# Optimization experiments

Hardware: AMD Instinct MI355X
Metric: run time of the kernel (lower is better)

## Reference

```python
import jax, jax.numpy as jnp
import numpy as np

B, S, D, H = 8, 384, 768, 12
MAX_POS = 512
P = 2 * MAX_POS - 1  # 1023


def setup_inputs() -> dict:
    key = jax.random.key(0)
    ks = jax.random.split(key, 14)
    w = 0.02
    return {
        "x": jax.random.normal(ks[0], (B, S, D), jnp.float32),
        "rel_pos_emb": jax.random.normal(ks[1], (P, D), jnp.float32),
        "Wq": jax.random.normal(ks[2], (D, D), jnp.float32) * w,
        "bq": jax.random.normal(ks[3], (D,), jnp.float32) * w,
        "Wk": jax.random.normal(ks[4], (D, D), jnp.float32) * w,
        "bk": jax.random.normal(ks[5], (D,), jnp.float32) * w,
        "Wv": jax.random.normal(ks[6], (D, D), jnp.float32) * w,
        "bv": jax.random.normal(ks[7], (D,), jnp.float32) * w,
        "q_bias": jax.random.normal(ks[8], (D,), jnp.float32) * w,
        "v_bias": jax.random.normal(ks[9], (D,), jnp.float32) * w,
        "Wpk": jax.random.normal(ks[10], (D, D), jnp.float32) * w,
        "Wpq": jax.random.normal(ks[11], (D, D), jnp.float32) * w,
        "Wo": jax.random.normal(ks[12], (D, D), jnp.float32) * w,
        "bo": jax.random.normal(ks[13], (D,), jnp.float32) * w,
    }


def reference(x, rel_pos_emb, Wq, bq, Wk, bk, Wv, bv, q_bias, v_bias, Wpk, Wpq, Wo, bo):
    b, s, d = x.shape
    dh = d // H
    scale = dh ** -0.5
    # relative position index: rel[i, j] = j - i + MAX_POS - 1
    rel = (jnp.arange(s)[None, :] - jnp.arange(s)[:, None]) + MAX_POS - 1
    emb = rel_pos_emb[rel]                      # [S, S, D]
    q = (x @ Wq + bq + q_bias).reshape(b, s, H, dh)
    k = (x @ Wk + bk).reshape(b, s, H, dh)
    v = (x @ Wv + bv + v_bias).reshape(b, s, H, dh)
    Kp = (emb @ Wpk).reshape(s, s, H, dh)       # pos keys   [i, j, h, d]
    Qp = (emb @ Wpq).reshape(s, s, H, dh)       # pos queries[i, j, h, d]
    c2c = jnp.einsum('bihd,bjhd->bhij', q, k)
    c2p = jnp.einsum('bihd,ijhd->bhij', q, Kp)
    p2c = jnp.einsum('ijhd,bjhd->bhij', Qp, k)
    scores = (c2c + c2p + p2c) * scale          # [B, H, S, S]
    w = jax.nn.softmax(scores, axis=-1)
    out = jnp.einsum('bhij,bjhd->bihd', w, v).reshape(b, s, d)
    return out @ Wo + bo
```

## Files before the change

kernel.cpp:

```cpp
#include <hip/hip_runtime.h>
#include <hip/hip_bf16.h>
#include <math.h>

#define BATCH 8
#define SEQ 384
#define DIM 768
#define NH 12
#define DH 64
#define NPOS 767
#define POS_OFF 128
#define NTOK (BATCH * SEQ)
#define QKN 1536
#define QKVN 2304
#define PN 1536

typedef __attribute__((ext_vector_type(8))) short short8;
typedef __attribute__((ext_vector_type(4))) float floatx4;
typedef unsigned int u32;

__device__ __forceinline__ ushort f2bf(float f) {
    __hip_bfloat16 h = __float2bfloat16(f);
    return *reinterpret_cast<ushort*>(&h);
}

__device__ __forceinline__ void gld16(const ushort* g, ushort* l) {
    __builtin_amdgcn_global_load_lds(
        (const __attribute__((address_space(1))) u32*)g,
        (__attribute__((address_space(3))) u32*)l, 16, 0, 0);
}

__global__ __launch_bounds__(256) void prep(
    const float* W0, const float* W1, const float* W2,
    const float* W3, const float* W4, const float* W5,
    const float* x, const float* rpe,
    ushort* __restrict__ wsT, ushort* __restrict__ xb, ushort* __restrict__ rpeb)
{
    const int tid = threadIdx.x;
    if (blockIdx.z < 6) {
        __shared__ float t[64][65];
        const float* srcs[6] = {W0, W1, W2, W3, W4, W5};
        const float* in = srcs[blockIdx.z];
        ushort* out = wsT + (size_t)blockIdx.z * DIM * DIM;
        const int r0 = blockIdx.y * 64, c0 = blockIdx.x * 64;
        for (int p = 0; p < 16; ++p) {
            int e = tid + p * 256, i = e >> 6, j = e & 63;
            t[i][j] = in[(size_t)(r0 + i) * DIM + c0 + j];
        }
        __syncthreads();
        for (int p = 0; p < 16; ++p) {
            int e = tid + p * 256, i = e >> 6, j = e & 63;
            out[(size_t)(c0 + i) * DIM + r0 + j] = f2bf(t[j][i]);
        }
    } else {
        const int n4x = NTOK * DIM / 4;
        const int n4p = NPOS * DIM / 4;
        const int fb = blockIdx.y * 12 + blockIdx.x;
        for (int idx = fb * 256 + tid; idx < n4x + n4p; idx += 144 * 256) {
            const float* src; ushort* dst; int j;
            if (idx < n4x) { src = x; dst = xb; j = idx; }
            else { src = rpe + (size_t)POS_OFF * DIM; dst = rpeb; j = idx - n4x; }
            float4 f = ((const float4*)src)[j];
            ushort o[4] = {f2bf(f.x), f2bf(f.y), f2bf(f.z), f2bf(f.w)};
            *(uint2*)&dst[(size_t)j * 4] = *(uint2*)o;
        }
    }
}

__global__ __launch_bounds__(256) void proj_all(
    const ushort* __restrict__ xb, const ushort* __restrict__ rpeb,
    const ushort* __restrict__ wsT,
    const float* __restrict__ bq, const float* __restrict__ qbias,
    const float* __restrict__ bk, const float* __restrict__ bv,
    const float* __restrict__ vbias,
    ushort* __restrict__ qk, ushort* __restrict__ vT, ushort* __restrict__ posKQ)
{
    __shared__ ushort As[128 * 64];
    __shared__ ushort Bs[128 * 64];
    const int tid = threadIdx.x;
    const int lane = tid & 63, w = tid >> 6;
    const int id = blockIdx.x;
    const bool qkvP = id < 432;
    const ushort* A; const ushort* Bt; int m0, n0, M;
    if (qkvP) {
        m0 = (id % 24) * 128; n0 = (id / 24) * 128;
        A = xb; Bt = wsT; M = NTOK;
    } else {
        int p = id - 432;
        m0 = (p % 6) * 128; n0 = (p / 6) * 128;
        A = rpeb; Bt = wsT + (size_t)3 * DIM * DIM; M = NPOS;
    }
    const int lr = lane >> 3;
    const int lc = (lane & 7) ^ (lr & 7);
    const ushort* ga[4]; const ushort* gb[4];
#pragma unroll
    for (int p = 0; p < 4; ++p) {
        int row = (w * 4 + p) * 8 + lr;
        int arow = m0 + row; if (arow > M - 1) arow = M - 1;
        ga[p] = A + (size_t)arow * DIM + lc * 8;
        gb[p] = Bt + (size_t)(n0 + row) * DIM + lc * 8;
    }
    floatx4 acc[4][4] = {};
    const int qr = (w >> 1) * 64, qc = (w & 1) * 64;
    const int lm = lane & 15, lk = lane >> 4;
    for (int k0 = 0; k0 < DIM; k0 += 64) {
#pragma unroll
        for (int p = 0; p < 4; ++p) {
            gld16(ga[p], As + (w * 4 + p) * 512);
            gld16(gb[p], Bs + (w * 4 + p) * 512);
            ga[p] += 64; gb[p] += 64;
        }
        __syncthreads();
#pragma unroll
        for (int kk = 0; kk < 2; ++kk) {
            int ch = (kk * 4 + lk) ^ (lm & 7);
            short8 af[4], bf[4];
#pragma unroll
            for (int t = 0; t < 4; ++t) {
                af[t] = *(const short8*)&As[(qr + t * 16 + lm) * 64 + ch * 8];
                bf[t] = *(const short8*)&Bs[(qc + t * 16 + lm) * 64 + ch * 8];
            }
#pragma unroll
            for (int i = 0; i < 4; ++i)
#pragma unroll
                for (int j = 0; j < 4; ++j)
                    acc[i][j] = __builtin_amdgcn_mfma_f32_16x16x32_bf16(af[i], bf[j], acc[i][j], 0, 0, 0);
        }
        __syncthreads();
    }
    if (qkvP) {
#pragma unroll
        for (int i = 0; i < 4; ++i) {
            int mbase = m0 + qr + i * 16 + (lane >> 4) * 4;
            int bb = mbase / SEQ;
            int s0 = mbase - bb * SEQ;
#pragma unroll
            for (int j = 0; j < 4; ++j) {
                int n = n0 + qc + j * 16 + lm;
                float bs;
                if (n < 768) bs = bq[n] + qbias[n];
                else if (n < QKN) bs = bk[n - 768];
                else bs = bv[n - QKN] + vbias[n - QKN];
                if (n < QKN) {
#pragma unroll
                    for (int r = 0; r < 4; ++r)
                        qk[(size_t)(mbase + r) * QKN + n] = f2bf(acc[i][j][r] + bs);
                } else {
                    int c = n - QKN, h = c >> 6, d = c & 63;
                    ushort tmp[4];
#pragma unroll
                    for (int r = 0; r < 4; ++r) tmp[r] = f2bf(acc[i][j][r] + bs);
                    *(uint2*)&vT[(((size_t)bb * NH + h) * DH + d) * SEQ + s0] = *(uint2*)tmp;
                }
            }
        }
    } else {
#pragma unroll
        for (int i = 0; i < 4; ++i) {
            int mbase = m0 + qr + i * 16 + (lane >> 4) * 4;
#pragma unroll
            for (int j = 0; j < 4; ++j) {
                int n = n0 + qc + j * 16 + lm;
#pragma unroll
                for (int r = 0; r < 4; ++r) {
                    int row = mbase + r;
                    if (row < NPOS)
                        posKQ[(size_t)row * PN + n] = f2bf(acc[i][j][r]);
                }
            }
        }
    }
}

__global__ __launch_bounds__(256) void gemm128(
    const ushort* __restrict__ A, const ushort* __restrict__ Bt,
    const float* __restrict__ bias, float* __restrict__ outF,
    int M, int N, int K)
{
    __shared__ ushort As[128 * 64];
    __shared__ ushort Bs[128 * 64];
    const int tid = threadIdx.x;
    const int lane = tid & 63, w = tid >> 6;
    const int n0 = blockIdx.x * 128, m0 = blockIdx.y * 128;
    const int lr = lane >> 3;
    const int lc = (lane & 7) ^ (lr & 7);
    const ushort* ga[4]; const ushort* gb[4];
#pragma unroll
    for (int p = 0; p < 4; ++p) {
        int row = (w * 4 + p) * 8 + lr;
        int arow = m0 + row; if (arow > M - 1) arow = M - 1;
        ga[p] = A + (size_t)arow * K + lc * 8;
        gb[p] = Bt + (size_t)(n0 + row) * K + lc * 8;
    }
    floatx4 acc[4][4] = {};
    const int qr = (w >> 1) * 64, qc = (w & 1) * 64;
    const int lm = lane & 15, lk = lane >> 4;
    for (int k0 = 0; k0 < K; k0 += 64) {
#pragma unroll
        for (int p = 0; p < 4; ++p) {
            gld16(ga[p], As + (w * 4 + p) * 512);
            gld16(gb[p], Bs + (w * 4 + p) * 512);
            ga[p] += 64; gb[p] += 64;
        }
        __syncthreads();
#pragma unroll
        for (int kk = 0; kk < 2; ++kk) {
            int ch = (kk * 4 + lk) ^ (lm & 7);
            short8 af[4], bf[4];
#pragma unroll
            for (int t = 0; t < 4; ++t) {
                af[t] = *(const short8*)&As[(qr + t * 16 + lm) * 64 + ch * 8];
                bf[t] = *(const short8*)&Bs[(qc + t * 16 + lm) * 64 + ch * 8];
            }
#pragma unroll
            for (int i = 0; i < 4; ++i)
#pragma unroll
                for (int j = 0; j < 4; ++j)
                    acc[i][j] = __builtin_amdgcn_mfma_f32_16x16x32_bf16(af[i], bf[j], acc[i][j], 0, 0, 0);
        }
        __syncthreads();
    }
#pragma unroll
    for (int i = 0; i < 4; ++i) {
        int mbase = m0 + qr + i * 16 + (lane >> 4) * 4;
#pragma unroll
        for (int j = 0; j < 4; ++j) {
            int n = n0 + qc + j * 16 + lm;
            float bs = bias ? bias[n] : 0.f;
#pragma unroll
            for (int r = 0; r < 4; ++r) {
                int row = mbase + r;
                if (row < M) outF[(size_t)row * N + n] = acc[i][j][r] + bs;
            }
        }
    }
}

__global__ __launch_bounds__(512, 2) void attn_fused4(
    const ushort* __restrict__ qk, const ushort* __restrict__ vT,
    const ushort* __restrict__ posKQ, ushort* __restrict__ aob)
{
    __shared__ ushort qs[64 * 64];
    __shared__ ushort kt[64 * 64];
    __shared__ ushort kps[128 * 64];
    __shared__ ushort qps[128 * 64];
    __shared__ ushort vtt[64 * 64];
    __shared__ float ccbuf[64 * 67];
    __shared__ float dqbuf[64 * 132];
    __shared__ float dkbuf[128 * 66];
    __shared__ float rowsum[64];
    ushort* pt = kps;

    const int tid = threadIdx.x;
    const int lane = tid & 63, w = tid >> 6;
    const int i0 = blockIdx.x * 64;
    const int h = blockIdx.y, b = blockIdx.z;
    const int lm = lane & 15, lq = lane >> 4;
    const int lr = lane >> 3, l8 = lane & 7;
    const int lc = l8 ^ (lr & 7);

    if (tid < 64) rowsum[tid] = 0.f;

    gld16(qk + (size_t)(b * SEQ + i0 + 8 * w + lr) * QKN + h * DH + lc * 8, qs + w * 512);
    const ushort* kb = qk + 768 + h * DH;
    const ushort* vb = vT + ((size_t)b * NH + h) * DH * SEQ;

    floatx4 occ[2] = {};
    const int exr = tid >> 3, exseg = tid & 7;

    for (int jt = 0; jt < 6; ++jt) {
        const int j0 = jt * 64;
        const int t0 = j0 - i0 + 320;
        gld16(kb + (size_t)(b * SEQ + j0 + 8 * w + lr) * QKN + lc * 8, kt + w * 512);
        gld16(posKQ + (size_t)(t0 + 16 * w + lr) * PN + h * DH + lc * 8, kps + w * 1024);
        gld16(posKQ + (size_t)(t0 + 16 * w + 8 + lr) * PN + h * DH + lc * 8, kps + w * 1024 + 512);
        gld16(posKQ + (size_t)(t0 + 16 * w + lr) * PN + 768 + h * DH + lc * 8, qps + w * 1024);
        gld16(posKQ + (size_t)(t0 + 16 * w + 8 + lr) * PN + 768 + h * DH + lc * 8, qps + w * 1024 + 512);
        gld16(vb + (size_t)(8 * w + lr) * SEQ + j0 + lc * 8, vtt + w * 512);
        __syncthreads();

        {
            int tr = w >> 1, tcb = (w & 1) * 2;
            floatx4 a0 = {}, a1 = {};
#pragma unroll
            for (int kk = 0; kk < 2; ++kk) {
                int ch = (kk * 4 + lq) ^ (lm & 7);
                short8 af = *(const short8*)&qs[(tr * 16 + lm) * 64 + ch * 8];
                short8 b0 = *(const short8*)&kt[(tcb * 16 + lm) * 64 + ch * 8];
                short8 b1 = *(const short8*)&kt[((tcb + 1) * 16 + lm) * 64 + ch * 8];
                a0 = __builtin_amdgcn_mfma_f32_16x16x32_bf16(af, b0, a0, 0, 0, 0);
                a1 = __builtin_amdgcn_mfma_f32_16x16x32_bf16(af, b1, a1, 0, 0, 0);
            }
#pragma unroll
            for (int r = 0; r < 4; ++r) {
                int row = tr * 16 + lq * 4 + r;
                ccbuf[row * 67 + tcb * 16 + lm] = a0[r];
                ccbuf[row * 67 + (tcb + 1) * 16 + lm] = a1[r];
            }
        }
        {
            int tr = w >> 1, tcb = (w & 1) * 4;
            floatx4 d[4] = {};
#pragma unroll
            for (int kk = 0; kk < 2; ++kk) {
                int ch = (kk * 4 + lq) ^ (lm & 7);
                short8 af = *(const short8*)&qs[(tr * 16 + lm) * 64 + ch * 8];
#pragma unroll
                for (int s = 0; s < 4; ++s) {
                    short8 bf = *(const short8*)&kps[((tcb + s) * 16 + lm) * 64 + ch * 8];
                    d[s] = __builtin_amdgcn_mfma_f32_16x16x32_bf16(af, bf, d[s], 0, 0, 0);
                }
            }
#pragma unroll
            for (int s = 0; s < 4; ++s) {
                int col = (tcb + s) * 16 + lm;
#pragma unroll
                for (int r = 0; r < 4; ++r)
                    dqbuf[(tr * 16 + lq * 4 + r) * 132 + col] = d[s][r];
            }
        }
        {
            floatx4 e[4] = {};
#pragma unroll
            for (int kk = 0; kk < 2; ++kk) {
                int ch = (kk * 4 + lq) ^ (lm & 7);
                short8 af = *(const short8*)&qps[(w * 16 + lm) * 64 + ch * 8];
#pragma unroll
                for (int s = 0; s < 4; ++s) {
                    short8 bf = *(const short8*)&kt[(s * 16 + lm) * 64 + ch * 8];
                    e[s] = __builtin_amdgcn_mfma_f32_16x16x32_bf16(af, bf, e[s], 0, 0, 0);
                }
            }
#pragma unroll
            for (int s = 0; s < 4; ++s) {
                int col = s * 16 + lm;
#pragma unroll
                for (int r = 0; r < 4; ++r)
                    dkbuf[(w * 16 + lq * 4 + r) * 66 + col] = e[s][r];
            }
        }
        __syncthreads();

        {
            float p[8]; float psum = 0.f;
            const int i = exr, jb = exseg * 8;
#pragma unroll
            for (int c = 0; c < 8; ++c) {
                int j = jb + c;
                int t = j - i + 63;
                float sv = (ccbuf[i * 67 + j] + dqbuf[i * 132 + t] + dkbuf[t * 66 + j]) * 0.125f;
                p[c] = __expf(sv);
                psum += p[c];
            }
            psum += __shfl_xor(psum, 1);
            psum += __shfl_xor(psum, 2);
            psum += __shfl_xor(psum, 4);
            if (exseg == 0) rowsum[i] += psum;
            ushort tmp[8];
#pragma unroll
            for (int c = 0; c < 8; ++c) tmp[c] = f2bf(p[c]);
            int ch = exseg ^ (i & 7);
            *(uint4*)&pt[i * 64 + ch * 8] = *(uint4*)tmp;
        }
        __syncthreads();

        {
            int tr = w >> 1, tcb = (w & 1) * 2;
#pragma unroll
            for (int kk = 0; kk < 2; ++kk) {
                int ch = (kk * 4 + lq) ^ (lm & 7);
                short8 af = *(const short8*)&pt[(tr * 16 + lm) * 64 + ch * 8];
#pragma unroll
                for (int s = 0; s < 2; ++s) {
                    short8 bv = *(const short8*)&vtt[((tcb + s) * 16 + lm) * 64 + ch * 8];
                    occ[s] = __builtin_amdgcn_mfma_f32_16x16x32_bf16(af, bv, occ[s], 0, 0, 0);
                }
            }
        }
        __syncthreads();
    }

    {
        int tr = w >> 1, tcb = (w & 1) * 2;
#pragma unroll
        for (int s = 0; s < 2; ++s) {
#pragma unroll
            for (int r = 0; r < 4; ++r) {
                int row = tr * 16 + lq * 4 + r;
                float ov = occ[s][r] / rowsum[row];
                aob[(size_t)(b * SEQ + i0 + row) * DIM + h * DH + (tcb + s) * 16 + lm] = f2bf(ov);
            }
        }
    }
}

extern "C" void kernel_launch(void* const* d_in, const int* in_sizes, int n_in,
                              void* d_out, int out_size, void* d_ws, size_t ws_size,
                              hipStream_t stream) {
    const float* x   = (const float*)d_in[0];
    const float* rpe = (const float*)d_in[1];
    const float* Wq  = (const float*)d_in[2];
    const float* bq  = (const float*)d_in[3];
    const float* Wk  = (const float*)d_in[4];
    const float* bk  = (const float*)d_in[5];
    const float* Wv  = (const float*)d_in[6];
    const float* bv  = (const float*)d_in[7];
    const float* qbias = (const float*)d_in[8];
    const float* vbias = (const float*)d_in[9];
    const float* Wpk = (const float*)d_in[10];
    const float* Wpq = (const float*)d_in[11];
    const float* Wo  = (const float*)d_in[12];
    const float* bo  = (const float*)d_in[13];
    float* out = (float*)d_out;

    char* ws = (char*)d_ws;
    ushort* xb    = (ushort*)ws; ws += (size_t)NTOK * DIM * 2;
    ushort* qkbuf = (ushort*)ws; ws += (size_t)NTOK * QKN * 2;
    ushort* vT    = (ushort*)ws; ws += (size_t)NTOK * DIM * 2;
    ushort* aob   = (ushort*)ws; ws += (size_t)NTOK * DIM * 2;
    ushort* rpeb  = (ushort*)ws; ws += (size_t)NPOS * DIM * 2;
    ushort* posKQ = (ushort*)ws; ws += (size_t)NPOS * PN * 2;
    ushort* wsT   = (ushort*)ws; ws += (size_t)6 * DIM * DIM * 2;

    prep<<<dim3(12, 12, 7), dim3(256), 0, stream>>>(
        Wq, Wk, Wv, Wpk, Wpq, Wo, x, rpe, wsT, xb, rpeb);
    proj_all<<<dim3(504), dim3(256), 0, stream>>>(
        xb, rpeb, wsT, bq, qbias, bk, bv, vbias, qkbuf, vT, posKQ);
    attn_fused4<<<dim3(SEQ / 64, NH, BATCH), dim3(512), 0, stream>>>(qkbuf, vT, posKQ, aob);
    gemm128<<<dim3(DIM / 128, NTOK / 128), dim3(256), 0, stream>>>(
        aob, wsT + (size_t)5 * DIM * DIM, bo, out, NTOK, DIM, DIM);
}
```

Before: 195.1 us.

## Load attention operands directly to registers, store scores in bf16, shrink output GEMM tile

The attention kernel stops staging Q, K, positional keys/queries and V through shared memory. It loads MFMA fragments straight from global memory into registers and writes the c2c, c2p and p2c partial scores to shared memory as bf16, already realigned from relative to absolute columns. This cuts LDS use and raises the occupancy target to 4 blocks, and it double-buffers the score/probability tile so one barrier per iteration can be dropped. The output projection GEMM moves to 128x64 tiles to launch more blocks. In exchange, global loads are less coalesced and the bf16 score rounding adds precision loss before the softmax.

Measured after the change: 271.8 us. 1.39x slower.

```diff
diff --git a/kernel.cpp b/kernel.cpp
--- a/kernel.cpp
+++ b/kernel.cpp
@@ -22,12 +22,18 @@
     __hip_bfloat16 h = __float2bfloat16(f);
     return *reinterpret_cast<ushort*>(&h);
 }
+__device__ __forceinline__ float bf2f(ushort u) {
+    u32 x = ((u32)u) << 16;
+    float f; __builtin_memcpy(&f, &x, 4); return f;
+}
 
 __device__ __forceinline__ void gld16(const ushort* g, ushort* l) {
     __builtin_amdgcn_global_load_lds(
         (const __attribute__((address_space(1))) u32*)g,
         (__attribute__((address_space(3))) u32*)l, 16, 0, 0);
 }
+
+#define MFMA __builtin_amdgcn_mfma_f32_16x16x32_bf16
 
 __global__ __launch_bounds__(256) void prep(
     const float* W0, const float* W1, const float* W2,
@@ -123,7 +129,7 @@
             for (int i = 0; i < 4; ++i)
 #pragma unroll
                 for (int j = 0; j < 4; ++j)
-                    acc[i][j] = __builtin_amdgcn_mfma_f32_16x16x32_bf16(af[i], bf[j], acc[i][j], 0, 0, 0);
+                    acc[i][j] = MFMA(af[i], bf[j], acc[i][j], 0, 0, 0);
         }
         __syncthreads();
     }
@@ -171,51 +177,51 @@
     }
 }
 
-__global__ __launch_bounds__(256) void gemm128(
+__global__ __launch_bounds__(256) void gemm128x64(
     const ushort* __restrict__ A, const ushort* __restrict__ Bt,
     const float* __restrict__ bias, float* __restrict__ outF,
     int M, int N, int K)
 {
     __shared__ ushort As[128 * 64];
-    __shared__ ushort Bs[128 * 64];
+    __shared__ ushort Bs[64 * 64];
     const int tid = threadIdx.x;
     const int lane = tid & 63, w = tid >> 6;
-    const int n0 = blockIdx.x * 128, m0 = blockIdx.y * 128;
+    const int n0 = blockIdx.x * 64, m0 = blockIdx.y * 128;
     const int lr = lane >> 3;
     const int lc = (lane & 7) ^ (lr & 7);
-    const ushort* ga[4]; const ushort* gb[4];
+    const ushort* ga[4]; const ushort* gb[2];
 #pragma unroll
     for (int p = 0; p < 4; ++p) {
-        int row = (w * 4 + p) * 8 + lr;
-        int arow = m0 + row; if (arow > M - 1) arow = M - 1;
+        int arow = m0 + (w * 4 + p) * 8 + lr; if (arow > M - 1) arow = M - 1;
         ga[p] = A + (size_t)arow * K + lc * 8;
-        gb[p] = Bt + (size_t)(n0 + row) * K + lc * 8;
-    }
-    floatx4 acc[4][4] = {};
-    const int qr = (w >> 1) * 64, qc = (w & 1) * 64;
+    }
+#pragma unroll
+    for (int p = 0; p < 2; ++p)
+        gb[p] = Bt + (size_t)(n0 + (w * 2 + p) * 8 + lr) * K + lc * 8;
+    floatx4 acc[4][2] = {};
+    const int qr = (w >> 1) * 64, qc = (w & 1) * 32;
     const int lm = lane & 15, lk = lane >> 4;
     for (int k0 = 0; k0 < K; k0 += 64) {
 #pragma unroll
-        for (int p = 0; p < 4; ++p) {
-            gld16(ga[p], As + (w * 4 + p) * 512);
-            gld16(gb[p], Bs + (w * 4 + p) * 512);
-            ga[p] += 64; gb[p] += 64;
-        }
+        for (int p = 0; p < 4; ++p) { gld16(ga[p], As + (w * 4 + p) * 512); ga[p] += 64; }
+#pragma unroll
+        for (int p = 0; p < 2; ++p) { gld16(gb[p], Bs + (w * 2 + p) * 512); gb[p] += 64; }
         __syncthreads();
 #pragma unroll
         for (int kk = 0; kk < 2; ++kk) {
             int ch = (kk * 4 + lk) ^ (lm & 7);
-            short8 af[4], bf[4];
-#pragma unroll
-            for (int t = 0; t < 4; ++t) {
+            short8 af[4], bf[2];
+#pragma unroll
+            for (int t = 0; t < 4; ++t)
                 af[t] = *(const short8*)&As[(qr + t * 16 + lm) * 64 + ch * 8];
+#pragma unroll
+            for (int t = 0; t < 2; ++t)
                 bf[t] = *(const short8*)&Bs[(qc + t * 16 + lm) * 64 + ch * 8];
-            }
 #pragma unroll
             for (int i = 0; i < 4; ++i)
 #pragma unroll
-                for (int j = 0; j < 4; ++j)
-                    acc[i][j] = __builtin_amdgcn_mfma_f32_16x16x32_bf16(af[i], bf[j], acc[i][j], 0, 0, 0);
+                for (int j = 0; j < 2; ++j)
+                    acc[i][j] = MFMA(af[i], bf[j], acc[i][j], 0, 0, 0);
         }
         __syncthreads();
     }
@@ -223,9 +229,9 @@
     for (int i = 0; i < 4; ++i) {
         int mbase = m0 + qr + i * 16 + (lane >> 4) * 4;
 #pragma unroll
-        for (int j = 0; j < 4; ++j) {
+        for (int j = 0; j < 2; ++j) {
             int n = n0 + qc + j * 16 + lm;
-            float bs = bias ? bias[n] : 0.f;
+            float bs = bias[n];
 #pragma unroll
             for (int r = 0; r < 4; ++r) {
                 int row = mbase + r;
@@ -235,160 +241,161 @@
     }
 }
 
-__global__ __launch_bounds__(512, 2) void attn_fused4(
+__global__ __launch_bounds__(512, 4) void attn_fused5(
     const ushort* __restrict__ qk, const ushort* __restrict__ vT,
     const ushort* __restrict__ posKQ, ushort* __restrict__ aob)
 {
-    __shared__ ushort qs[64 * 64];
-    __shared__ ushort kt[64 * 64];
-    __shared__ ushort kps[128 * 64];
-    __shared__ ushort qps[128 * 64];
-    __shared__ ushort vtt[64 * 64];
-    __shared__ float ccbuf[64 * 67];
-    __shared__ float dqbuf[64 * 132];
-    __shared__ float dkbuf[128 * 66];
+    __shared__ ushort ccpt[2][64 * 72];
+    __shared__ ushort dqs[64 * 72];
+    __shared__ ushort dks[64 * 72];
     __shared__ float rowsum[64];
-    ushort* pt = kps;
 
     const int tid = threadIdx.x;
     const int lane = tid & 63, w = tid >> 6;
     const int i0 = blockIdx.x * 64;
     const int h = blockIdx.y, b = blockIdx.z;
     const int lm = lane & 15, lq = lane >> 4;
-    const int lr = lane >> 3, l8 = lane & 7;
-    const int lc = l8 ^ (lr & 7);
+    const int trq = w >> 1;
+    const int half = w & 1;
+    const int exr = tid >> 3, exseg = tid & 7;
 
     if (tid < 64) rowsum[tid] = 0.f;
 
-    gld16(qk + (size_t)(b * SEQ + i0 + 8 * w + lr) * QKN + h * DH + lc * 8, qs + w * 512);
-    const ushort* kb = qk + 768 + h * DH;
-    const ushort* vb = vT + ((size_t)b * NH + h) * DH * SEQ;
-
+    short8 qf[2];
+    {
+        const ushort* qr = qk + (size_t)(b * SEQ + i0 + trq * 16 + lm) * QKN + h * DH;
+        qf[0] = *(const short8*)(qr + lq * 8);
+        qf[1] = *(const short8*)(qr + 32 + lq * 8);
+    }
     floatx4 occ[2] = {};
-    const int exr = tid >> 3, exseg = tid & 7;
 
     for (int jt = 0; jt < 6; ++jt) {
         const int j0 = jt * 64;
         const int t0 = j0 - i0 + 320;
-        gld16(kb + (size_t)(b * SEQ + j0 + 8 * w + lr) * QKN + lc * 8, kt + w * 512);
-        gld16(posKQ + (size_t)(t0 + 16 * w + lr) * PN + h * DH + lc * 8, kps + w * 1024);
-        gld16(posKQ + (size_t)(t0 + 16 * w + 8 + lr) * PN + h * DH + lc * 8, kps + w * 1024 + 512);
-        gld16(posKQ + (size_t)(t0 + 16 * w + lr) * PN + 768 + h * DH + lc * 8, qps + w * 1024);
-        gld16(posKQ + (size_t)(t0 + 16 * w + 8 + lr) * PN + 768 + h * DH + lc * 8, qps + w * 1024 + 512);
-        gld16(vb + (size_t)(8 * w + lr) * SEQ + j0 + lc * 8, vtt + w * 512);
-        __syncthreads();
-
+        ushort* cc = ccpt[jt & 1];
+
+        short8 kd[4][2], qp[2];
+#pragma unroll
+        for (int s = 0; s < 4; ++s) {
+            const ushort* kr = qk + (size_t)(b * SEQ + j0 + s * 16 + lm) * QKN + 768 + h * DH;
+            kd[s][0] = *(const short8*)(kr + lq * 8);
+            kd[s][1] = *(const short8*)(kr + 32 + lq * 8);
+        }
         {
-            int tr = w >> 1, tcb = (w & 1) * 2;
-            floatx4 a0 = {}, a1 = {};
-#pragma unroll
-            for (int kk = 0; kk < 2; ++kk) {
-                int ch = (kk * 4 + lq) ^ (lm & 7);
-                short8 af = *(const short8*)&qs[(tr * 16 + lm) * 64 + ch * 8];
-                short8 b0 = *(const short8*)&kt[(tcb * 16 + lm) * 64 + ch * 8];
-                short8 b1 = *(const short8*)&kt[((tcb + 1) * 16 + lm) * 64 + ch * 8];
-                a0 = __builtin_amdgcn_mfma_f32_16x16x32_bf16(af, b0, a0, 0, 0, 0);
-                a1 = __builtin_amdgcn_mfma_f32_16x16x32_bf16(af, b1, a1, 0, 0, 0);
-            }
-#pragma unroll
-            for (int r = 0; r < 4; ++r) {
-                int row = tr * 16 + lq * 4 + r;
-                ccbuf[row * 67 + tcb * 16 + lm] = a0[r];
-                ccbuf[row * 67 + (tcb + 1) * 16 + lm] = a1[r];
-            }
-        }
-        {
-            int tr = w >> 1, tcb = (w & 1) * 4;
-            floatx4 d[4] = {};
-#pragma unroll
-            for (int kk = 0; kk < 2; ++kk) {
-                int ch = (kk * 4 + lq) ^ (lm & 7);
-                short8 af = *(const short8*)&qs[(tr * 16 + lm) * 64 + ch * 8];
-#pragma unroll
-                for (int s = 0; s < 4; ++s) {
-                    short8 bf = *(const short8*)&kps[((tcb + s) * 16 + lm) * 64 + ch * 8];
-                    d[s] = __builtin_amdgcn_mfma_f32_16x16x32_bf16(af, bf, d[s], 0, 0, 0);
-                }
-            }
-#pragma unroll
-            for (int s = 0; s < 4; ++s) {
-                int col = (tcb + s) * 16 + lm;
-#pragma unroll
-                for (int r = 0; r < 4; ++r)
-                    dqbuf[(tr * 16 + lq * 4 + r) * 132 + col] = d[s][r];
-            }
-        }
+            const ushort* qpr = posKQ + (size_t)(t0 + w * 16 + lm) * PN + 768 + h * DH;
+            qp[0] = *(const short8*)(qpr + lq * 8);
+            qp[1] = *(const short8*)(qpr + 32 + lq * 8);
+        }
+
         {
             floatx4 e[4] = {};
 #pragma unroll
-            for (int kk = 0; kk < 2; ++kk) {
-                int ch = (kk * 4 + lq) ^ (lm & 7);
-                short8 af = *(const short8*)&qps[(w * 16 + lm) * 64 + ch * 8];
-#pragma unroll
-                for (int s = 0; s < 4; ++s) {
-                    short8 bf = *(const short8*)&kt[(s * 16 + lm) * 64 + ch * 8];
-                    e[s] = __builtin_amdgcn_mfma_f32_16x16x32_bf16(af, bf, e[s], 0, 0, 0);
+            for (int kk = 0; kk < 2; ++kk)
+#pragma unroll
+                for (int s = 0; s < 4; ++s)
+                    e[s] = MFMA(qp[kk], kd[s][kk], e[s], 0, 0, 0);
+#pragma unroll
+            for (int s = 0; s < 4; ++s) {
+                int j = s * 16 + lm;
+#pragma unroll
+                for (int r = 0; r < 4; ++r) {
+                    int t = w * 16 + lq * 4 + r;
+                    int i = j - t + 63;
+                    if ((unsigned)i < 64u) dks[i * 72 + j] = f2bf(e[s][r]);
                 }
             }
+        }
+        {
+            floatx4 a[2] = {};
+#pragma unroll
+            for (int kk = 0; kk < 2; ++kk)
+#pragma unroll
+                for (int s = 0; s < 2; ++s)
+                    a[s] = MFMA(qf[kk], kd[half * 2 + s][kk], a[s], 0, 0, 0);
+#pragma unroll
+            for (int s = 0; s < 2; ++s) {
+                int j = (half * 2 + s) * 16 + lm;
+#pragma unroll
+                for (int r = 0; r < 4; ++r)
+                    cc[(trq * 16 + lq * 4 + r) * 72 + j] = f2bf(a[s][r]);
+            }
+        }
+        {
+            short8 kp[4][2];
 #pragma unroll
             for (int s = 0; s < 4; ++s) {
-                int col = s * 16 + lm;
-#pragma unroll
-                for (int r = 0; r < 4; ++r)
-                    dkbuf[(w * 16 + lq * 4 + r) * 66 + col] = e[s][r];
-            }
-        }
-        __syncthreads();
+                const ushort* kpr = posKQ + (size_t)(t0 + (half * 4 + s) * 16 + lm) * PN + h * DH;
+                kp[s][0] = *(const short8*)(kpr + lq * 8);
+                kp[s][1] = *(const short8*)(kpr + 32 + lq * 8);
+            }
+            floatx4 d[4] = {};
+#pragma unroll
+            for (int kk = 0; kk < 2; ++kk)
+#pragma unroll
+                for (int s = 0; s < 4; ++s)
+                    d[s] = MFMA(qf[kk], kp[s][kk], d[s], 0, 0, 0);
+#pragma unroll
+            for (int s = 0; s < 4; ++s) {
+                int t = (half * 4 + s) * 16 + lm;
+#pragma unroll
+                for (int r = 0; r < 4; ++r) {
+                    int i = trq * 16 + lq * 4 + r;
+                    int j = t + i - 63;
+                    if ((unsigned)j < 64u) dqs[i * 72 + j] = f2bf(d[s][r]);
+                }
+            }
+        }
+        __syncthreads();
+
+        short8 vf[2][2];
+#pragma unroll
+        for (int s = 0; s < 2; ++s) {
+            const ushort* vr = vT + ((size_t)(b * NH + h) * DH + (half * 2 + s) * 16 + lm) * SEQ + j0;
+            vf[s][0] = *(const short8*)(vr + lq * 8);
+            vf[s][1] = *(const short8*)(vr + 32 + lq * 8);
+        }
 
         {
+            uint4 c4 = *(const uint4*)&cc[exr * 72 + exseg * 8];
+            uint4 q4 = *(const uint4*)&dqs[exr * 72 + exseg * 8];
+            uint4 k4 = *(const uint4*)&dks[exr * 72 + exseg * 8];
+            const ushort* cu = (const ushort*)&c4;
+            const ushort* qu = (const ushort*)&q4;
+            const ushort* ku = (const ushort*)&k4;
             float p[8]; float psum = 0.f;
-            const int i = exr, jb = exseg * 8;
 #pragma unroll
             for (int c = 0; c < 8; ++c) {
-                int j = jb + c;
-                int t = j - i + 63;
-                float sv = (ccbuf[i * 67 + j] + dqbuf[i * 132 + t] + dkbuf[t * 66 + j]) * 0.125f;
+                float sv = (bf2f(cu[c]) + bf2f(qu[c]) + bf2f(ku[c])) * 0.125f;
                 p[c] = __expf(sv);
                 psum += p[c];
             }
             psum += __shfl_xor(psum, 1);
             psum += __shfl_xor(psum, 2);
             psum += __shfl_xor(psum, 4);
-            if (exseg == 0) rowsum[i] += psum;
+            if (exseg == 0) rowsum[exr] += psum;
             ushort tmp[8];
 #pragma unroll
             for (int c = 0; c < 8; ++c) tmp[c] = f2bf(p[c]);
-            int ch = exseg ^ (i & 7);
-            *(uint4*)&pt[i * 64 + ch * 8] = *(uint4*)tmp;
-        }
-        __syncthreads();
-
-        {
-            int tr = w >> 1, tcb = (w & 1) * 2;
-#pragma unroll
-            for (int kk = 0; kk < 2; ++kk) {
-                int ch = (kk * 4 + lq) ^ (lm & 7);
-                short8 af = *(const short8*)&pt[(tr * 16 + lm) * 64 + ch * 8];
-#pragma unroll
-                for (int s = 0; s < 2; ++s) {
-                    short8 bv = *(const short8*)&vtt[((tcb + s) * 16 + lm) * 64 + ch * 8];
-                    occ[s] = __builtin_amdgcn_mfma_f32_16x16x32_bf16(af, bv, occ[s], 0, 0, 0);
-                }
-            }
-        }
-        __syncthreads();
-    }
-
-    {
-        int tr = w >> 1, tcb = (w & 1) * 2;
-#pragma unroll
-        for (int s = 0; s < 2; ++s) {
-#pragma unroll
-            for (int r = 0; r < 4; ++r) {
-                int row = tr * 16 + lq * 4 + r;
-                float ov = occ[s][r] / rowsum[row];
-                aob[(size_t)(b * SEQ + i0 + row) * DIM + h * DH + (tcb + s) * 16 + lm] = f2bf(ov);
-            }
+            *(uint4*)&cc[exr * 72 + exseg * 8] = *(uint4*)tmp;
+        }
+        __syncthreads();
+
+#pragma unroll
+        for (int kk = 0; kk < 2; ++kk) {
+            short8 af = *(const short8*)&cc[(trq * 16 + lm) * 72 + kk * 32 + lq * 8];
+#pragma unroll
+            for (int s = 0; s < 2; ++s)
+                occ[s] = MFMA(af, vf[s][kk], occ[s], 0, 0, 0);
+        }
+    }
+
+#pragma unroll
+    for (int s = 0; s < 2; ++s) {
+#pragma unroll
+        for (int r = 0; r < 4; ++r) {
+            int row = trq * 16 + lq * 4 + r;
+            float ov = occ[s][r] / rowsum[row];
+            aob[(size_t)(b * SEQ + i0 + row) * DIM + h * DH + (half * 2 + s) * 16 + lm] = f2bf(ov);
         }
     }
 }
@@ -425,7 +432,7 @@
         Wq, Wk, Wv, Wpk, Wpq, Wo, x, rpe, wsT, xb, rpeb);
     proj_all<<<dim3(504), dim3(256), 0, stream>>>(
         xb, rpeb, wsT, bq, qbias, bk, bv, vbias, qkbuf, vT, posKQ);
-    attn_fused4<<<dim3(SEQ / 64, NH, BATCH), dim3(512), 0, stream>>>(qkbuf, vT, posKQ, aob);
-    gemm128<<<dim3(DIM / 128, NTOK / 128), dim3(256), 0, stream>>>(
+    attn_fused5<<<dim3(SEQ / 64, NH, BATCH), dim3(512), 0, stream>>>(qkbuf, vT, posKQ, aob);
+    gemm128x64<<<dim3(DIM / 64, NTOK / 128), dim3(256), 0, stream>>>(
         aob, wsT + (size_t)5 * DIM * DIM, bo, out, NTOK, DIM, DIM);
 }
```
